# Performance work log

Hardware: AMD Instinct MI355X
Metric: run time of the kernel (lower is better)

The kernel has to match this reference:

```python
import jax, jax.numpy as jnp
import numpy as np

N_NODES = 50000
N_EDGES = 800000
NDIM_IN = 128
EDIM_IN = 128
NDIM_OUT = 128
EDIM_OUT = 128


def setup_inputs() -> dict:
    key = jax.random.key(0)
    ks = jax.random.split(key, 8)
    nfeats = jax.random.normal(ks[0], (N_NODES, NDIM_IN), dtype=jnp.float32)
    efeats = jax.random.normal(ks[1], (N_EDGES, EDIM_IN), dtype=jnp.float32)
    u = jax.random.randint(ks[2], (N_EDGES,), 0, N_NODES, dtype=jnp.int32)
    v = jax.random.randint(ks[3], (N_EDGES,), 0, N_NODES, dtype=jnp.int32)
    # torch.nn.Linear params: weight [out, in], bias [out]
    d_apply_in = 2 * NDIM_IN + EDIM_IN  # concat(nfeats, h_neigh)
    lim1 = 1.0 / np.sqrt(d_apply_in)
    W_apply_w = jax.random.uniform(ks[4], (NDIM_OUT, d_apply_in), jnp.float32, -lim1, lim1)
    W_apply_b = jax.random.uniform(ks[5], (NDIM_OUT,), jnp.float32, -lim1, lim1)
    lim2 = 1.0 / np.sqrt(2 * NDIM_OUT)
    W_edge_w = jax.random.uniform(ks[6], (EDIM_OUT, 2 * NDIM_OUT), jnp.float32, -lim2, lim2)
    W_edge_b = jax.random.uniform(ks[7], (EDIM_OUT,), jnp.float32, -lim2, lim2)
    return {"nfeats": nfeats, "efeats": efeats, "u": u, "v": v,
            "W_apply_w": W_apply_w, "W_apply_b": W_apply_b,
            "W_edge_w": W_edge_w, "W_edge_b": W_edge_b}


def reference(nfeats, efeats, u, v, W_apply_w, W_apply_b, W_edge_w, W_edge_b):
    n_nodes = nfeats.shape[0]
    # message per edge: concat(src node h, edge h)  -> [E, ndim_in+edim_in]
    msg = jnp.concatenate([nfeats[u], efeats], axis=1)
    # mean reduction over incoming edges at dst node v (0 for isolated nodes, like DGL)
    sums = jax.ops.segment_sum(msg, v, num_segments=n_nodes)
    counts = jax.ops.segment_sum(jnp.ones((msg.shape[0],), msg.dtype), v, num_segments=n_nodes)
    h_neigh = jnp.where(counts[:, None] > 0, sums / jnp.maximum(counts, 1.0)[:, None], 0.0)
    # node update
    h_nodes_new = jnp.concatenate([nfeats, h_neigh], axis=1) @ W_apply_w.T + W_apply_b
    h_nodes_new = jax.nn.relu(h_nodes_new)
    # edge update
    edge_input = jnp.concatenate([h_nodes_new[u], h_nodes_new[v]], axis=1)
    h_edges_new = jax.nn.relu(edge_input @ W_edge_w.T + W_edge_b)
    return h_nodes_new, h_edges_new
```

## Files before the change

### kernel.cpp

```cpp
#include <hip/hip_runtime.h>
#include <hip/hip_bf16.h>

#define N_NODES_C 50000
#define N_EDGES_C 800000
#define NBLK_NODES 196
#define EDGE_HEAD_ROWS 50048

typedef __attribute__((ext_vector_type(8))) short bf16x8;
typedef __attribute__((ext_vector_type(4))) float f32x4;

__device__ __forceinline__ unsigned short f2bf(float f) {
    unsigned int x = __float_as_uint(f);
    unsigned int r = x + 0x7fffu + ((x >> 16) & 1u);
    return (unsigned short)(r >> 16);
}
__device__ __forceinline__ float bf2f(unsigned short s) {
    return __uint_as_float(((unsigned int)s) << 16);
}

__global__ __launch_bounds__(256) void zero_k(int* __restrict__ cnt)
{
    int i = blockIdx.x * 256 + threadIdx.x;
    if (i < N_NODES_C) cnt[i] = 0;
}

__global__ __launch_bounds__(256) void count_k(const int* __restrict__ v, int* __restrict__ cnt)
{
    int e = blockIdx.x * 256 + threadIdx.x;
    atomicAdd(&cnt[v[e]], 1);
}

__global__ __launch_bounds__(256) void scan_partial_k(
    const int* __restrict__ cnt, int* __restrict__ bsum)
{
    __shared__ int ws[4];
    int b = blockIdx.x, t = threadIdx.x, lane = t & 63, wid = t >> 6;
    int i = b * 256 + t;
    int x = (i < N_NODES_C) ? cnt[i] : 0;
    int s = x;
#pragma unroll
    for (int d = 1; d < 64; d <<= 1) {
        int tv = __shfl_up(s, d, 64);
        if (lane >= d) s += tv;
    }
    if (lane == 63) ws[wid] = s;
    __syncthreads();
    if (t == 0) bsum[b] = ws[0] + ws[1] + ws[2] + ws[3];
}

__global__ __launch_bounds__(256) void scan_block_k(
    const int* __restrict__ bsum, int* __restrict__ boff, int* __restrict__ rowst)
{
    __shared__ int ws[4];
    int t = threadIdx.x, lane = t & 63, wid = t >> 6;
    int x = (t < NBLK_NODES) ? bsum[t] : 0;
    int s = x;
#pragma unroll
    for (int d = 1; d < 64; d <<= 1) {
        int tv = __shfl_up(s, d, 64);
        if (lane >= d) s += tv;
    }
    if (lane == 63) ws[wid] = s;
    __syncthreads();
    if (t == 0) {
        int a = 0;
#pragma unroll
        for (int w = 0; w < 4; ++w) { int tmp = ws[w]; ws[w] = a; a += tmp; }
    }
    __syncthreads();
    int excl = ws[wid] + s - x;
    if (t < NBLK_NODES) boff[t] = excl;
    if (t == 255) rowst[N_NODES_C] = excl;
}

__global__ __launch_bounds__(256) void scan_scatter_k(
    const int* __restrict__ cnt, const int* __restrict__ boff,
    int* __restrict__ rowst, int* __restrict__ cursor)
{
    __shared__ int ws[4];
    int b = blockIdx.x, t = threadIdx.x, lane = t & 63, wid = t >> 6;
    int i = b * 256 + t;
    int x = (i < N_NODES_C) ? cnt[i] : 0;
    int s = x;
#pragma unroll
    for (int d = 1; d < 64; d <<= 1) {
        int tv = __shfl_up(s, d, 64);
        if (lane >= d) s += tv;
    }
    if (lane == 63) ws[wid] = s;
    __syncthreads();
    if (t == 0) {
        int a = 0;
#pragma unroll
        for (int w = 0; w < 4; ++w) { int tmp = ws[w]; ws[w] = a; a += tmp; }
    }
    __syncthreads();
    int excl = boff[b] + ws[wid] + s - x;
    if (i < N_NODES_C) { rowst[i] = excl; cursor[i] = excl; }
}

__global__ __launch_bounds__(256) void fill_k(const int* __restrict__ v,
                                              const int* __restrict__ u,
                                              int* __restrict__ cursor,
                                              int2* __restrict__ pairs)
{
    int e = blockIdx.x * 256 + threadIdx.x;
    int pos = atomicAdd(&cursor[v[e]], 1);
    pairs[pos] = make_int2(e, u[e]);
}

__global__ __launch_bounds__(256) void aggregate_k(
    const int2* __restrict__ pairs, const int* __restrict__ rowst,
    const float* __restrict__ nfeats, const float* __restrict__ efeats,
    float* __restrict__ h_neigh)
{
    __shared__ float4 red[256];
    int n = blockIdx.x, tid = threadIdx.x;
    int grp = tid >> 6, lane = tid & 63;
    int s = rowst[n], e_end = rowst[n + 1];
    int deg = e_end - s;

    float4 acc = make_float4(0.f, 0.f, 0.f, 0.f);
    float4 acc2 = make_float4(0.f, 0.f, 0.f, 0.f);
    int i = s + grp;
    for (; i + 4 < e_end; i += 8) {
        int2 pA = pairs[i];
        int2 pB = pairs[i + 4];
        const float* srcA = (lane < 32)
            ? (nfeats + (size_t)pA.y * 128 + lane * 4)
            : (efeats + (size_t)pA.x * 128 + (lane - 32) * 4);
        const float* srcB = (lane < 32)
            ? (nfeats + (size_t)pB.y * 128 + lane * 4)
            : (efeats + (size_t)pB.x * 128 + (lane - 32) * 4);
        float4 a4 = *reinterpret_cast<const float4*>(srcA);
        float4 b4 = *reinterpret_cast<const float4*>(srcB);
        acc.x += a4.x; acc.y += a4.y; acc.z += a4.z; acc.w += a4.w;
        acc2.x += b4.x; acc2.y += b4.y; acc2.z += b4.z; acc2.w += b4.w;
    }
    if (i < e_end) {
        int2 p = pairs[i];
        const float* src = (lane < 32)
            ? (nfeats + (size_t)p.y * 128 + lane * 4)
            : (efeats + (size_t)p.x * 128 + (lane - 32) * 4);
        float4 vv = *reinterpret_cast<const float4*>(src);
        acc.x += vv.x; acc.y += vv.y; acc.z += vv.z; acc.w += vv.w;
    }
    acc.x += acc2.x; acc.y += acc2.y; acc.z += acc2.z; acc.w += acc2.w;
    red[tid] = acc;
    __syncthreads();
    if (grp == 0) {
        float4 a = red[lane], b = red[64 + lane], c = red[128 + lane], d = red[192 + lane];
        float r = (deg > 0) ? 1.f / (float)deg : 0.f;
        float4 o;
        o.x = (a.x + b.x + c.x + d.x) * r;
        o.y = (a.y + b.y + c.y + d.y) * r;
        o.z = (a.z + b.z + c.z + d.z) * r;
        o.w = (a.w + b.w + c.w + d.w) * r;
        *reinterpret_cast<float4*>(h_neigh + (size_t)n * 256 + lane * 4) = o;
    }
}

__device__ __forceinline__ void stage_half_row(
    const float* __restrict__ src, char* __restrict__ lds, int row, int halfg)
{
#pragma unroll
    for (int g = 0; g < 4; ++g) {
        float4 f0 = reinterpret_cast<const float4*>(src)[g * 2 + 0];
        float4 f1 = reinterpret_cast<const float4*>(src)[g * 2 + 1];
        union { unsigned short s[8]; uint4 q; } pk;
        pk.s[0] = f2bf(f0.x); pk.s[1] = f2bf(f0.y);
        pk.s[2] = f2bf(f0.z); pk.s[3] = f2bf(f0.w);
        pk.s[4] = f2bf(f1.x); pk.s[5] = f2bf(f1.y);
        pk.s[6] = f2bf(f1.z); pk.s[7] = f2bf(f1.w);
        int byteoff = ((halfg * 4 + g) * 16) ^ ((row & 7) << 4);
        *reinterpret_cast<uint4*>(lds + row * 128 + byteoff) = pk.q;
    }
}

__device__ __forceinline__ void mfma_slab(
    const char* __restrict__ Xs, const char* __restrict__ Ws,
    int wm, int wn, int lane, f32x4 (&acc)[4][4])
{
#pragma unroll
    for (int c = 0; c < 2; ++c) {
        int kb = c * 64 + (lane >> 4) * 16;
        bf16x8 a[4], b[4];
#pragma unroll
        for (int i = 0; i < 4; ++i) {
            int row = wm * 64 + i * 16 + (lane & 15);
            a[i] = *reinterpret_cast<const bf16x8*>(
                Xs + row * 128 + (kb ^ ((row & 7) << 4)));
        }
#pragma unroll
        for (int j = 0; j < 4; ++j) {
            int row = wn * 64 + j * 16 + (lane & 15);
            b[j] = *reinterpret_cast<const bf16x8*>(
                Ws + row * 128 + (kb ^ ((row & 7) << 4)));
        }
#pragma unroll
        for (int i = 0; i < 4; ++i)
#pragma unroll
            for (int j = 0; j < 4; ++j)
                acc[i][j] = __builtin_amdgcn_mfma_f32_16x16x32_bf16(
                    a[i], b[j], acc[i][j], 0, 0, 0);
    }
}

__device__ __forceinline__ void epilogue_store(
    const f32x4 (&acc)[4][4], const float* __restrict__ bias,
    float* __restrict__ out, int row_base, int row_limit, int wm, int wn, int lane)
{
    int col0 = wn * 64 + (lane & 15);
    int row0 = row_base + wm * 64 + (lane >> 4) * 4;
#pragma unroll
    for (int j = 0; j < 4; ++j) {
        float bj = bias[col0 + j * 16];
#pragma unroll
        for (int i = 0; i < 4; ++i) {
#pragma unroll
            for (int r = 0; r < 4; ++r) {
                int row = row0 + i * 16 + r;
                if (row < row_limit) {
                    float val = fmaxf(acc[i][j][r] + bj, 0.f);
                    out[(size_t)row * 128 + col0 + j * 16] = val;
                }
            }
        }
    }
}

__global__ __launch_bounds__(256) void node_k(
    const float* __restrict__ nfeats, const float* __restrict__ h_neigh,
    const float* __restrict__ W, const float* __restrict__ bias,
    float* __restrict__ out)
{
    __shared__ uint4 XsBuf[1024];
    __shared__ uint4 WsBuf[1024];
    char* Xs = (char*)XsBuf;
    char* Ws = (char*)WsBuf;

    int tid = threadIdx.x;
    int n0  = blockIdx.x * 128;
    int wave = tid >> 6, lane = tid & 63;
    int wm = wave >> 1, wn = wave & 1;
    int srow = tid >> 1, shalf = tid & 1;

    int nrow = n0 + srow;
    if (nrow >= N_NODES_C) nrow = N_NODES_C - 1;

    f32x4 acc[4][4];
#pragma unroll
    for (int i = 0; i < 4; ++i)
#pragma unroll
        for (int j = 0; j < 4; ++j) acc[i][j] = (f32x4)0.f;

#pragma unroll
    for (int k0 = 0; k0 < 384; k0 += 64) {
        const float* xsrc = (k0 < 128)
            ? (nfeats  + (size_t)nrow * 128 + k0         + shalf * 32)
            : (h_neigh + (size_t)nrow * 256 + (k0 - 128) + shalf * 32);
        stage_half_row(xsrc, Xs, srow, shalf);
        const float* wsrc = W + (size_t)srow * 384 + k0 + shalf * 32;
        stage_half_row(wsrc, Ws, srow, shalf);
        __syncthreads();
        mfma_slab(Xs, Ws, wm, wn, lane, acc);
        __syncthreads();
    }

    epilogue_store(acc, bias, out, n0, N_NODES_C, wm, wn, lane);
}

__global__ __launch_bounds__(256) void pp_k(
    const float* __restrict__ h, const float* __restrict__ W,
    unsigned short* __restrict__ P)
{
    __shared__ uint4 XsBuf[1024];
    __shared__ uint4 WsBuf[1024];
    char* Xs = (char*)XsBuf;
    char* Ws = (char*)WsBuf;

    int tid = threadIdx.x;
    int n0  = blockIdx.x * 128;
    int cb  = blockIdx.y;
    int wave = tid >> 6, lane = tid & 63;
    int wm = wave >> 1, wn = wave & 1;
    int srow = tid >> 1, shalf = tid & 1;

    int nrow = n0 + srow;
    if (nrow >= N_NODES_C) nrow = N_NODES_C - 1;

    f32x4 acc[4][4];
#pragma unroll
    for (int i = 0; i < 4; ++i)
#pragma unroll
        for (int j = 0; j < 4; ++j) acc[i][j] = (f32x4)0.f;

#pragma unroll
    for (int k0 = 0; k0 < 128; k0 += 64) {
        const float* xsrc = h + (size_t)nrow * 128 + k0 + shalf * 32;
        stage_half_row(xsrc, Xs, srow, shalf);
        const float* wsrc = W + (size_t)srow * 256 + cb * 128 + k0 + shalf * 32;
        stage_half_row(wsrc, Ws, srow, shalf);
        __syncthreads();
        mfma_slab(Xs, Ws, wm, wn, lane, acc);
        __syncthreads();
    }

    int col0 = wn * 64 + (lane & 15);
    int row0 = n0 + wm * 64 + (lane >> 4) * 4;
#pragma unroll
    for (int j = 0; j < 4; ++j) {
#pragma unroll
        for (int i = 0; i < 4; ++i) {
#pragma unroll
            for (int r = 0; r < 4; ++r) {
                int row = row0 + i * 16 + r;
                if (row < N_NODES_C)
                    P[(size_t)row * 256 + cb * 128 + col0 + j * 16] = f2bf(acc[i][j][r]);
            }
        }
    }
}

__global__ __launch_bounds__(256) void edge_add_k(
    const unsigned short* __restrict__ P, const int* __restrict__ u,
    const int* __restrict__ v, const float* __restrict__ bias,
    float* __restrict__ out, int e_base)
{
    int c = blockIdx.x * 256 + threadIdx.x;
    int e = e_base + (c >> 5);
    int q = c & 31;
    int uu = u[e], vv = v[e];
    ushort4 pa = *reinterpret_cast<const ushort4*>(P + (size_t)uu * 256 + q * 4);
    ushort4 pb = *reinterpret_cast<const ushort4*>(P + (size_t)vv * 256 + 128 + q * 4);
    float4 b4 = *reinterpret_cast<const float4*>(bias + q * 4);
    float4 o;
    o.x = fmaxf(bf2f(pa.x) + bf2f(pb.x) + b4.x, 0.f);
    o.y = fmaxf(bf2f(pa.y) + bf2f(pb.y) + b4.y, 0.f);
    o.z = fmaxf(bf2f(pa.z) + bf2f(pb.z) + b4.z, 0.f);
    o.w = fmaxf(bf2f(pa.w) + bf2f(pb.w) + b4.w, 0.f);
    *reinterpret_cast<float4*>(out + (size_t)e * 128 + q * 4) = o;
}

__global__ __launch_bounds__(256) void edge_head_k(
    const float* __restrict__ h, const int* __restrict__ u,
    const int* __restrict__ v, const float* __restrict__ W,
    const float* __restrict__ bias, float* __restrict__ out)
{
    __shared__ uint4 XsBuf[1024];
    __shared__ uint4 WsBuf[1024];
    __shared__ int us[128], vs[128];
    char* Xs = (char*)XsBuf;
    char* Ws = (char*)WsBuf;

    int tid = threadIdx.x;
    int e0  = blockIdx.x * 128;
    if (tid < 128) us[tid]       = u[e0 + tid];
    else           vs[tid - 128] = v[e0 + tid - 128];
    __syncthreads();

    int wave = tid >> 6, lane = tid & 63;
    int wm = wave >> 1, wn = wave & 1;
    int srow = tid >> 1, shalf = tid & 1;

    f32x4 acc[4][4];
#pragma unroll
    for (int i = 0; i < 4; ++i)
#pragma unroll
        for (int j = 0; j < 4; ++j) acc[i][j] = (f32x4)0.f;

#pragma unroll
    for (int k0 = 0; k0 < 256; k0 += 64) {
        int node = (k0 < 128) ? us[srow] : vs[srow];
        const float* xsrc = h + (size_t)node * 128 + (k0 & 127) + shalf * 32;
        stage_half_row(xsrc, Xs, srow, shalf);
        const float* wsrc = W + (size_t)srow * 256 + k0 + shalf * 32;
        stage_half_row(wsrc, Ws, srow, shalf);
        __syncthreads();
        mfma_slab(Xs, Ws, wm, wn, lane, acc);
        __syncthreads();
    }

    epilogue_store(acc, bias, out, e0, N_EDGES_C, wm, wn, lane);
}

extern "C" void kernel_launch(void* const* d_in, const int* in_sizes, int n_in,
                              void* d_out, int out_size, void* d_ws, size_t ws_size,
                              hipStream_t stream)
{
    const float* nfeats    = (const float*)d_in[0];
    const float* efeats    = (const float*)d_in[1];
    const int*   u         = (const int*)d_in[2];
    const int*   v         = (const int*)d_in[3];
    const float* W_apply_w = (const float*)d_in[4];
    const float* W_apply_b = (const float*)d_in[5];
    const float* W_edge_w  = (const float*)d_in[6];
    const float* W_edge_b  = (const float*)d_in[7];

    float* out      = (float*)d_out;
    float* h_nodes  = out;
    float* edge_out = out + (size_t)N_NODES_C * 128;

    float* scratch = edge_out;
    float* h_neigh = scratch;
    int*   cnt     = (int*)(scratch + 12800000);
    int*   rowst   = cnt + N_NODES_C;
    int*   cursor  = rowst + N_NODES_C + 1;
    int2*  pairs   = (int2*)(cursor + N_NODES_C + 2);
    int*   bsum    = (int*)(pairs + N_EDGES_C);
    int*   boff    = bsum + 256;

    const size_t P_ELEMS = (size_t)N_NODES_C * 256;
    bool p_in_ws = ws_size >= P_ELEMS * sizeof(unsigned short);
    unsigned short* P = p_in_ws ? (unsigned short*)d_ws
                                : (unsigned short*)edge_out;

    zero_k<<<NBLK_NODES, 256, 0, stream>>>(cnt);
    count_k<<<N_EDGES_C / 256, 256, 0, stream>>>(v, cnt);
    scan_partial_k<<<NBLK_NODES, 256, 0, stream>>>(cnt, bsum);
    scan_block_k<<<1, 256, 0, stream>>>(bsum, boff, rowst);
    scan_scatter_k<<<NBLK_NODES, 256, 0, stream>>>(cnt, boff, rowst, cursor);
    fill_k<<<N_EDGES_C / 256, 256, 0, stream>>>(v, u, cursor, pairs);
    aggregate_k<<<N_NODES_C, 256, 0, stream>>>(pairs, rowst, nfeats, efeats, h_neigh);

    node_k<<<(N_NODES_C + 127) / 128, 256, 0, stream>>>(
        nfeats, h_neigh, W_apply_w, W_apply_b, h_nodes);

    pp_k<<<dim3((N_NODES_C + 127) / 128, 2), 256, 0, stream>>>(
        h_nodes, W_edge_w, P);

    if (p_in_ws) {
        edge_add_k<<<N_EDGES_C * 32 / 256, 256, 0, stream>>>(
            P, u, v, W_edge_b, edge_out, 0);
    } else {
        edge_add_k<<<(N_EDGES_C - EDGE_HEAD_ROWS) * 32 / 256, 256, 0, stream>>>(
            P, u, v, W_edge_b, edge_out, EDGE_HEAD_ROWS);
        edge_head_k<<<EDGE_HEAD_ROWS / 128, 256, 0, stream>>>(
            h_nodes, u, v, W_edge_w, W_edge_b, edge_out);
    }
}
```

Measured before the change: 448.9 us.

## Aggregate one node per wave, store neighbor mean and weights as bf16

The aggregation kernel now gives each node a single wavefront instead of a 256-thread block. That removes the LDS reduction and the block barrier, and unrolls the edge loop four ways. The neighbor mean is written as bf16, halving the h_neigh write and the node GEMM's read. A new prep kernel converts both weight matrices to bf16 once so the GEMMs can copy them straight into LDS without per-block conversion. The trade-offs are an extra launch and less parallelism per high-degree node.

```diff
diff --git a/kernel.cpp b/kernel.cpp
--- a/kernel.cpp
+++ b/kernel.cpp
@@ -112,52 +112,55 @@
 __global__ __launch_bounds__(256) void aggregate_k(
     const int2* __restrict__ pairs, const int* __restrict__ rowst,
     const float* __restrict__ nfeats, const float* __restrict__ efeats,
-    float* __restrict__ h_neigh)
-{
-    __shared__ float4 red[256];
-    int n = blockIdx.x, tid = threadIdx.x;
-    int grp = tid >> 6, lane = tid & 63;
-    int s = rowst[n], e_end = rowst[n + 1];
+    unsigned short* __restrict__ hnb)
+{
+    int wv   = blockIdx.x * 4 + (threadIdx.x >> 6);
+    int lane = threadIdx.x & 63;
+    if (wv >= N_NODES_C) return;
+    int s = rowst[wv], e_end = rowst[wv + 1];
     int deg = e_end - s;
 
-    float4 acc = make_float4(0.f, 0.f, 0.f, 0.f);
-    float4 acc2 = make_float4(0.f, 0.f, 0.f, 0.f);
-    int i = s + grp;
-    for (; i + 4 < e_end; i += 8) {
-        int2 pA = pairs[i];
-        int2 pB = pairs[i + 4];
-        const float* srcA = (lane < 32)
-            ? (nfeats + (size_t)pA.y * 128 + lane * 4)
-            : (efeats + (size_t)pA.x * 128 + (lane - 32) * 4);
-        const float* srcB = (lane < 32)
-            ? (nfeats + (size_t)pB.y * 128 + lane * 4)
-            : (efeats + (size_t)pB.x * 128 + (lane - 32) * 4);
-        float4 a4 = *reinterpret_cast<const float4*>(srcA);
-        float4 b4 = *reinterpret_cast<const float4*>(srcB);
-        acc.x += a4.x; acc.y += a4.y; acc.z += a4.z; acc.w += a4.w;
-        acc2.x += b4.x; acc2.y += b4.y; acc2.z += b4.z; acc2.w += b4.w;
-    }
-    if (i < e_end) {
+    float4 a0 = make_float4(0.f, 0.f, 0.f, 0.f);
+    float4 a1 = a0, a2 = a0, a3 = a0;
+    int i = s;
+    for (; i + 3 < e_end; i += 4) {
+        int2 p0 = pairs[i + 0];
+        int2 p1 = pairs[i + 1];
+        int2 p2 = pairs[i + 2];
+        int2 p3 = pairs[i + 3];
+        const float* s0 = (lane < 32) ? (nfeats + (size_t)p0.y * 128 + lane * 4)
+                                      : (efeats + (size_t)p0.x * 128 + (lane - 32) * 4);
+        const float* s1 = (lane < 32) ? (nfeats + (size_t)p1.y * 128 + lane * 4)
+                                      : (efeats + (size_t)p1.x * 128 + (lane - 32) * 4);
+        const float* s2 = (lane < 32) ? (nfeats + (size_t)p2.y * 128 + lane * 4)
+                                      : (efeats + (size_t)p2.x * 128 + (lane - 32) * 4);
+        const float* s3 = (lane < 32) ? (nfeats + (size_t)p3.y * 128 + lane * 4)
+                                      : (efeats + (size_t)p3.x * 128 + (lane - 32) * 4);
+        float4 v0 = *reinterpret_cast<const float4*>(s0);
+        float4 v1 = *reinterpret_cast<const float4*>(s1);
+        float4 v2 = *reinterpret_cast<const float4*>(s2);
+        float4 v3 = *reinterpret_cast<const float4*>(s3);
+        a0.x += v0.x; a0.y += v0.y; a0.z += v0.z; a0.w += v0.w;
+        a1.x += v1.x; a1.y += v1.y; a1.z += v1.z; a1.w += v1.w;
+        a2.x += v2.x; a2.y += v2.y; a2.z += v2.z; a2.w += v2.w;
+        a3.x += v3.x; a3.y += v3.y; a3.z += v3.z; a3.w += v3.w;
+    }
+    for (; i < e_end; ++i) {
         int2 p = pairs[i];
-        const float* src = (lane < 32)
-            ? (nfeats + (size_t)p.y * 128 + lane * 4)
-            : (efeats + (size_t)p.x * 128 + (lane - 32) * 4);
+        const float* src = (lane < 32) ? (nfeats + (size_t)p.y * 128 + lane * 4)
+                                       : (efeats + (size_t)p.x * 128 + (lane - 32) * 4);
         float4 vv = *reinterpret_cast<const float4*>(src);
-        acc.x += vv.x; acc.y += vv.y; acc.z += vv.z; acc.w += vv.w;
-    }
-    acc.x += acc2.x; acc.y += acc2.y; acc.z += acc2.z; acc.w += acc2.w;
-    red[tid] = acc;
-    __syncthreads();
-    if (grp == 0) {
-        float4 a = red[lane], b = red[64 + lane], c = red[128 + lane], d = red[192 + lane];
-        float r = (deg > 0) ? 1.f / (float)deg : 0.f;
-        float4 o;
-        o.x = (a.x + b.x + c.x + d.x) * r;
-        o.y = (a.y + b.y + c.y + d.y) * r;
-        o.z = (a.z + b.z + c.z + d.z) * r;
-        o.w = (a.w + b.w + c.w + d.w) * r;
-        *reinterpret_cast<float4*>(h_neigh + (size_t)n * 256 + lane * 4) = o;
-    }
+        a0.x += vv.x; a0.y += vv.y; a0.z += vv.z; a0.w += vv.w;
+    }
+    a0.x += a1.x + a2.x + a3.x;
+    a0.y += a1.y + a2.y + a3.y;
+    a0.z += a1.z + a2.z + a3.z;
+    a0.w += a1.w + a2.w + a3.w;
+    float r = (deg > 0) ? 1.f / (float)deg : 0.f;
+    ushort4 o;
+    o.x = f2bf(a0.x * r); o.y = f2bf(a0.y * r);
+    o.z = f2bf(a0.z * r); o.w = f2bf(a0.w * r);
+    *reinterpret_cast<ushort4*>(hnb + (size_t)wv * 256 + lane * 4) = o;
 }
 
 __device__ __forceinline__ void stage_half_row(
@@ -177,6 +180,17 @@
     }
 }
 
+__device__ __forceinline__ void stage_half_row_cp(
+    const unsigned short* __restrict__ src, char* __restrict__ lds, int row, int halfg)
+{
+#pragma unroll
+    for (int g = 0; g < 4; ++g) {
+        uint4 q = reinterpret_cast<const uint4*>(src)[g];
+        int byteoff = ((halfg * 4 + g) * 16) ^ ((row & 7) << 4);
+        *reinterpret_cast<uint4*>(lds + row * 128 + byteoff) = q;
+    }
+}
+
 __device__ __forceinline__ void mfma_slab(
     const char* __restrict__ Xs, const char* __restrict__ Ws,
     int wm, int wn, int lane, f32x4 (&acc)[4][4])
@@ -229,9 +243,18 @@
     }
 }
 
+__global__ __launch_bounds__(256) void prep_w_k(
+    const float* __restrict__ Wa, const float* __restrict__ We,
+    unsigned short* __restrict__ wa, unsigned short* __restrict__ we)
+{
+    int i = blockIdx.x * 256 + threadIdx.x;
+    if (i < 49152)      wa[i] = f2bf(Wa[i]);
+    else if (i < 81920) we[i - 49152] = f2bf(We[i - 49152]);
+}
+
 __global__ __launch_bounds__(256) void node_k(
-    const float* __restrict__ nfeats, const float* __restrict__ h_neigh,
-    const float* __restrict__ W, const float* __restrict__ bias,
+    const float* __restrict__ nfeats, const unsigned short* __restrict__ hnb,
+    const unsigned short* __restrict__ wa, const float* __restrict__ bias,
     float* __restrict__ out)
 {
     __shared__ uint4 XsBuf[1024];
@@ -256,12 +279,14 @@
 
 #pragma unroll
     for (int k0 = 0; k0 < 384; k0 += 64) {
-        const float* xsrc = (k0 < 128)
-            ? (nfeats  + (size_t)nrow * 128 + k0         + shalf * 32)
-            : (h_neigh + (size_t)nrow * 256 + (k0 - 128) + shalf * 32);
-        stage_half_row(xsrc, Xs, srow, shalf);
-        const float* wsrc = W + (size_t)srow * 384 + k0 + shalf * 32;
-        stage_half_row(wsrc, Ws, srow, shalf);
+        if (k0 < 128)
+            stage_half_row(nfeats + (size_t)nrow * 128 + k0 + shalf * 32,
+                           Xs, srow, shalf);
+        else
+            stage_half_row_cp(hnb + (size_t)nrow * 256 + (k0 - 128) + shalf * 32,
+                              Xs, srow, shalf);
+        stage_half_row_cp(wa + (size_t)srow * 384 + k0 + shalf * 32,
+                          Ws, srow, shalf);
         __syncthreads();
         mfma_slab(Xs, Ws, wm, wn, lane, acc);
         __syncthreads();
@@ -271,7 +296,7 @@
 }
 
 __global__ __launch_bounds__(256) void pp_k(
-    const float* __restrict__ h, const float* __restrict__ W,
+    const float* __restrict__ h, const unsigned short* __restrict__ we,
     unsigned short* __restrict__ P)
 {
     __shared__ uint4 XsBuf[1024];
@@ -297,10 +322,9 @@
 
 #pragma unroll
     for (int k0 = 0; k0 < 128; k0 += 64) {
-        const float* xsrc = h + (size_t)nrow * 128 + k0 + shalf * 32;
-        stage_half_row(xsrc, Xs, srow, shalf);
-        const float* wsrc = W + (size_t)srow * 256 + cb * 128 + k0 + shalf * 32;
-        stage_half_row(wsrc, Ws, srow, shalf);
+        stage_half_row(h + (size_t)nrow * 128 + k0 + shalf * 32, Xs, srow, shalf);
+        stage_half_row_cp(we + (size_t)srow * 256 + cb * 128 + k0 + shalf * 32,
+                          Ws, srow, shalf);
         __syncthreads();
         mfma_slab(Xs, Ws, wm, wn, lane, acc);
         __syncthreads();
@@ -372,10 +396,10 @@
 #pragma unroll
     for (int k0 = 0; k0 < 256; k0 += 64) {
         int node = (k0 < 128) ? us[srow] : vs[srow];
-        const float* xsrc = h + (size_t)node * 128 + (k0 & 127) + shalf * 32;
-        stage_half_row(xsrc, Xs, srow, shalf);
-        const float* wsrc = W + (size_t)srow * 256 + k0 + shalf * 32;
-        stage_half_row(wsrc, Ws, srow, shalf);
+        stage_half_row(h + (size_t)node * 128 + (k0 & 127) + shalf * 32,
+                       Xs, srow, shalf);
+        stage_half_row(W + (size_t)srow * 256 + k0 + shalf * 32,
+                       Ws, srow, shalf);
         __syncthreads();
         mfma_slab(Xs, Ws, wm, wn, lane, acc);
         __syncthreads();
@@ -401,14 +425,15 @@
     float* h_nodes  = out;
     float* edge_out = out + (size_t)N_NODES_C * 128;
 
-    float* scratch = edge_out;
-    float* h_neigh = scratch;
-    int*   cnt     = (int*)(scratch + 12800000);
+    unsigned short* hnb = (unsigned short*)edge_out;
+    int*   cnt     = (int*)(edge_out + 6400000);
     int*   rowst   = cnt + N_NODES_C;
     int*   cursor  = rowst + N_NODES_C + 1;
     int2*  pairs   = (int2*)(cursor + N_NODES_C + 2);
     int*   bsum    = (int*)(pairs + N_EDGES_C);
     int*   boff    = bsum + 256;
+    unsigned short* wa = (unsigned short*)(boff + 256);
+    unsigned short* we = wa + 49152;
 
     const size_t P_ELEMS = (size_t)N_NODES_C * 256;
     bool p_in_ws = ws_size >= P_ELEMS * sizeof(unsigned short);
@@ -416,18 +441,19 @@
                                 : (unsigned short*)edge_out;
 
     zero_k<<<NBLK_NODES, 256, 0, stream>>>(cnt);
+    prep_w_k<<<320, 256, 0, stream>>>(W_apply_w, W_edge_w, wa, we);
     count_k<<<N_EDGES_C / 256, 256, 0, stream>>>(v, cnt);
     scan_partial_k<<<NBLK_NODES, 256, 0, stream>>>(cnt, bsum);
     scan_block_k<<<1, 256, 0, stream>>>(bsum, boff, rowst);
     scan_scatter_k<<<NBLK_NODES, 256, 0, stream>>>(cnt, boff, rowst, cursor);
     fill_k<<<N_EDGES_C / 256, 256, 0, stream>>>(v, u, cursor, pairs);
-    aggregate_k<<<N_NODES_C, 256, 0, stream>>>(pairs, rowst, nfeats, efeats, h_neigh);
+    aggregate_k<<<N_NODES_C / 4, 256, 0, stream>>>(pairs, rowst, nfeats, efeats, hnb);
 
     node_k<<<(N_NODES_C + 127) / 128, 256, 0, stream>>>(
-        nfeats, h_neigh, W_apply_w, W_apply_b, h_nodes);
+        nfeats, hnb, wa, W_apply_b, h_nodes);
 
     pp_k<<<dim3((N_NODES_C + 127) / 128, 2), 256, 0, stream>>>(
-        h_nodes, W_edge_w, P);
+        h_nodes, we, P);
 
     if (p_in_ws) {
         edge_add_k<<<N_EDGES_C * 32 / 256, 256, 0, stream>>>(
```

Result: faster. 415.4 us (-7.5%).
